# Kernel tuning notes

Hardware: AMD Instinct MI355X
Metric: run time of the kernel (lower is better)

Reference implementation:

```python
import jax, jax.numpy as jnp
import numpy as np

D_MODEL = 1024
NUM_HEADS = 16
HEAD_DIM = D_MODEL // NUM_HEADS  # 64
ROPE_THETA = 10000.0
SEQ_LEN = 4096
BATCH = 1


def apply_rope(x, positions, theta=ROPE_THETA):
    # x: [b, h, s, d], positions: [s]
    d = x.shape[-1]
    inv_freq = theta ** (-jnp.arange(0, d, 2, dtype=jnp.float32) / d)  # [d/2]
    angles = positions.astype(jnp.float32)[:, None] * inv_freq[None, :]  # [s, d/2]
    cos = jnp.cos(angles)  # [s, d/2]
    sin = jnp.sin(angles)
    x1 = x[..., 0::2]  # [b, h, s, d/2]
    x2 = x[..., 1::2]
    r1 = x1 * cos - x2 * sin
    r2 = x1 * sin + x2 * cos
    # interleave back to [..., d]
    out = jnp.stack([r1, r2], axis=-1).reshape(x.shape)
    return out.astype(x.dtype)


def setup_inputs() -> dict:
    key = jax.random.key(0)
    k_x, k_qkv, k_o = jax.random.split(key, 3)
    scale_in = 1.0 / np.sqrt(D_MODEL)
    return {
        "x": jax.random.normal(k_x, (BATCH, SEQ_LEN, D_MODEL), dtype=jnp.float32),
        "token_positions": jnp.arange(SEQ_LEN, dtype=jnp.int64 if jax.config.jax_enable_x64 else jnp.int32),
        "w_qkv": jax.random.normal(k_qkv, (3 * D_MODEL, D_MODEL), dtype=jnp.float32) * scale_in,
        "w_o": jax.random.normal(k_o, (D_MODEL, D_MODEL), dtype=jnp.float32) * scale_in,
    }


def reference(x, token_positions, w_qkv, w_o):
    b, s, _ = x.shape
    # QKV projection (Linear without bias, weight [out, in])
    x_qkv = jnp.einsum('bsd,ed->bse', x, w_qkv)  # [b, s, 3*d_model]
    # rearrange 'b s (three heads kv) -> three b heads s kv'
    x_qkv = x_qkv.reshape(b, s, 3, NUM_HEADS, HEAD_DIM)
    x_qkv = jnp.transpose(x_qkv, (2, 0, 3, 1, 4))  # [3, b, h, s, d]
    q, k, v = x_qkv[0], x_qkv[1], x_qkv[2]
    q = apply_rope(q, token_positions)
    k = apply_rope(k, token_positions)
    # scaled dot-product attention with causal mask
    scores = jnp.einsum('bhnd,bhmd->bhnm', q, k) / jnp.sqrt(jnp.float32(HEAD_DIM))
    causal = jnp.tril(jnp.ones((s, s), dtype=bool))  # [s, s]
    scores = jnp.where(causal[None, None], scores, jnp.float32(-jnp.inf))
    weights = jax.nn.softmax(scores, axis=-1)
    attn = jnp.einsum('bhnm,bhmd->bhnd', weights, v)  # [b, h, s, d]
    attn = jnp.transpose(attn, (0, 2, 1, 3)).reshape(b, s, NUM_HEADS * HEAD_DIM)
    return jnp.einsum('bsd,ed->bse', attn, w_o)
```

## Files before the change

### kernel.cpp

```cpp
#include <hip/hip_runtime.h>

#define SEQ 4096
#define DMODEL 1024
#define HEADS 16
#define HD 64
#define NQKV 3072

typedef __attribute__((ext_vector_type(8))) __bf16 bf16x8;
typedef __attribute__((ext_vector_type(4))) __bf16 bf16x4;
typedef __attribute__((ext_vector_type(8))) short short8;
typedef __attribute__((ext_vector_type(4))) float f32x4;

__device__ __forceinline__ unsigned short f2bf(float f) {
    unsigned u = __builtin_bit_cast(unsigned, f);
    return (unsigned short)((u + 0x7fffu + ((u >> 16) & 1u)) >> 16);
}
__device__ __forceinline__ float bf2f(unsigned short h) {
    return __builtin_bit_cast(float, (unsigned)h << 16);
}

__device__ __forceinline__ void gload16(const void* g, void* l) {
    __builtin_amdgcn_global_load_lds(
        (const __attribute__((address_space(1))) unsigned int*)g,
        (__attribute__((address_space(3))) unsigned int*)l, 16, 0, 0);
}

#define TS(qt, kh) (0x40 | ((kh) << 5) | (qt))
__device__ __constant__ unsigned char TASKS[48] = {
    TS(31,0), TS(31,1), TS(30,0), 15,
    TS(30,1), TS(29,0), TS(29,1), TS(28,0), 14,
    TS(28,1), TS(27,0), TS(27,1), TS(26,0), 13,
    TS(26,1), TS(25,0), TS(25,1), TS(24,0), 12,
    TS(24,1), TS(23,0), TS(23,1), TS(22,0), 11,
    TS(22,1), TS(21,0), TS(21,1), TS(20,0), 10,
    TS(20,1), TS(19,0), TS(19,1), TS(18,0), 9,
    TS(18,1), TS(17,0), TS(17,1), TS(16,0), 8,
    TS(16,1), 7,
    6, 5, 4, 3, 2, 1, 0
};

__global__ void f2bf_all(const float* __restrict__ x, const float* __restrict__ wqkv,
                         const float* __restrict__ wo, unsigned short* __restrict__ dst) {
    const int N0 = SEQ * DMODEL / 4;
    const int N1 = N0 + NQKV * DMODEL / 4;
    const int NT = N1 + DMODEL * DMODEL / 4;
    int i = blockIdx.x * 256 + threadIdx.x;
    int stride = gridDim.x * 256;
    for (; i < NT; i += stride) {
        const float4* src;
        if (i < N0)      src = reinterpret_cast<const float4*>(x) + i;
        else if (i < N1) src = reinterpret_cast<const float4*>(wqkv) + (i - N0);
        else             src = reinterpret_cast<const float4*>(wo) + (i - N1);
        float4 f = *src;
        ushort4 o;
        o.x = f2bf(f.x); o.y = f2bf(f.y); o.z = f2bf(f.z); o.w = f2bf(f.w);
        reinterpret_cast<ushort4*>(dst)[i] = o;
    }
}

template <int EPI>
__global__ __launch_bounds__(256) void gemm_bt(const unsigned short* __restrict__ A,
                                               const unsigned short* __restrict__ B,
                                               float* __restrict__ outF,
                                               unsigned short* __restrict__ outB,
                                               int M, int N, int K) {
    alignas(16) __shared__ unsigned short a_lds[2][128 * 32];
    alignas(16) __shared__ unsigned short b_lds[2][128 * 32];
    const int tid = threadIdx.x;
    const int wave = tid >> 6, lane = tid & 63;
    const int l16 = lane & 15, g = lane >> 4;
    const int wr = wave >> 1, wc = wave & 1;
    const int bm = blockIdx.x, bn = blockIdx.y;

    const int lrow = lane >> 2;
    const int lcol = (lane & 3) * 8;

    const unsigned short* Ag = A + (size_t)(bm * 128 + lrow) * K + lcol;
    const unsigned short* Bg = B + (size_t)(bn * 128 + lrow) * K + lcol;

    f32x4 acc[4][4] = {};
    const int NS = K / 32;

    auto STAGE = [&](int b, int ks) {
#pragma unroll
        for (int j = 0; j < 2; ++j) {
            int chunk = wave * 2 + j;
            gload16(Ag + (size_t)(chunk * 16) * K + ks * 32, a_lds[b] + chunk * 512);
            gload16(Bg + (size_t)(chunk * 16) * K + ks * 32, b_lds[b] + chunk * 512);
        }
    };

    STAGE(0, 0);

    for (int ks = 0; ks < NS; ++ks) {
        const int cur = ks & 1;
        asm volatile("s_waitcnt vmcnt(0)" ::: "memory");
        __builtin_amdgcn_s_barrier();
        if (ks + 1 < NS) STAGE(cur ^ 1, ks + 1);

        bf16x8 af[4], bfr[4];
#pragma unroll
        for (int m = 0; m < 4; ++m)
            af[m] = *reinterpret_cast<const bf16x8*>(a_lds[cur] + (wr * 64 + m * 16 + l16) * 32 + g * 8);
#pragma unroll
        for (int n = 0; n < 4; ++n)
            bfr[n] = *reinterpret_cast<const bf16x8*>(b_lds[cur] + (wc * 64 + n * 16 + l16) * 32 + g * 8);
        __builtin_amdgcn_s_setprio(1);
#pragma unroll
        for (int m = 0; m < 4; ++m)
#pragma unroll
            for (int n = 0; n < 4; ++n)
                acc[m][n] = __builtin_amdgcn_mfma_f32_16x16x32_bf16(af[m], bfr[n], acc[m][n], 0, 0, 0);
        __builtin_amdgcn_s_setprio(0);
    }

#pragma unroll
    for (int m = 0; m < 4; ++m)
#pragma unroll
        for (int n = 0; n < 4; ++n)
#pragma unroll
            for (int r = 0; r < 4; ++r) {
                int row = bm * 128 + wr * 64 + m * 16 + g * 4 + r;
                int col = bn * 128 + wc * 64 + n * 16 + l16;
                float v = acc[m][n][r];
                if (EPI == 0) {
                    int part = col >> 10;
                    int hd = col & 1023;
                    int h = hd >> 6, d = hd & 63;
                    outB[(size_t)((part * HEADS + h) * SEQ + row) * HD + d] = f2bf(v);
                } else {
                    outF[(size_t)row * N + col] = v;
                }
            }
}

__global__ __launch_bounds__(256) void rope_kernel(unsigned short* qkv, const int* __restrict__ pos) {
    int idx = blockIdx.x * 256 + threadIdx.x;
    int chunk = idx & 7;
    int row = idx >> 3;
    int s = row & (SEQ - 1);
    int ph = row >> 12;
    float p = (float)pos[s];
    float scale = (ph < HEADS) ? 0.125f * 1.4426950408889634f : 1.0f;
    unsigned short* base = qkv + ((size_t)ph * SEQ + s) * HD + chunk * 8;
    short8 v = *reinterpret_cast<short8*>(base);
    short8 o;
    const float k = -13.287712379549449f / 32.0f;
#pragma unroll
    for (int j = 0; j < 4; ++j) {
        int i = chunk * 4 + j;
        float ang = p * exp2f((float)i * k);
        float sn, cs;
        sincosf(ang, &sn, &cs);
        float x1 = bf2f((unsigned short)v[2 * j]);
        float x2 = bf2f((unsigned short)v[2 * j + 1]);
        o[2 * j]     = (short)f2bf((x1 * cs - x2 * sn) * scale);
        o[2 * j + 1] = (short)f2bf((x1 * sn + x2 * cs) * scale);
    }
    *reinterpret_cast<short8*>(base) = o;
}

__global__ __launch_bounds__(256) void transpose_v(const unsigned short* __restrict__ qkv,
                                                   unsigned short* __restrict__ vt) {
    const int st = blockIdx.x;
    const int h = blockIdx.y;
    __shared__ unsigned short tile[64][72];
    const unsigned short* Vg = qkv + (size_t)((2 * HEADS + h) * SEQ) * HD;
    const int tid = threadIdx.x;
#pragma unroll
    for (int j = 0; j < 2; ++j) {
        int b = (tid + j * 256) * 8;
        int row = b >> 6;
        int col = b & 63;
        short8 v = *reinterpret_cast<const short8*>(Vg + (size_t)(st * 64 + row) * HD + col);
#pragma unroll
        for (int i = 0; i < 8; ++i) tile[row][col + i] = (unsigned short)v[i];
    }
    __syncthreads();
#pragma unroll
    for (int j = 0; j < 2; ++j) {
        int b = (tid + j * 256) * 8;
        int d = b >> 6;
        int sc = b & 63;
        short8 o;
#pragma unroll
        for (int i = 0; i < 8; ++i) o[i] = (short)tile[sc + i][d];
        *reinterpret_cast<short8*>(vt + (size_t)(h * HD + d) * SEQ + st * 64 + sc) = o;
    }
}

__global__ __launch_bounds__(512) void attn_kernel(const unsigned short* __restrict__ qkv,
                                                   const unsigned short* __restrict__ vt,
                                                   unsigned short* __restrict__ attnout,
                                                   unsigned short* __restrict__ pO,
                                                   float* __restrict__ lmf) {
    const int bid = blockIdx.x;
    const int xcd = bid & 7;
    const int slot = bid >> 3;
    const int hloc = slot & 1;
    const unsigned char e = TASKS[slot >> 1];
    const int qtile = e & 31;
    const int khalf = (e >> 5) & 1;
    const bool isSplit = (e >> 6) != 0;
    const int T = qtile + 1, Hh = (T + 1) >> 1;
    const int k0 = isSplit ? (khalf ? Hh : 0) : 0;
    const int k1 = isSplit ? (khalf ? T : Hh) : T;
    const int h = xcd * 2 + hloc;

    const int tid = threadIdx.x;
    const int wave = tid >> 6, lane = tid & 63;
    const int l16 = lane & 15, g = lane >> 4;

    alignas(16) __shared__ unsigned short k_lds[2][128 * 64];
    alignas(16) __shared__ unsigned short v_lds[2][2][64 * 64];
    alignas(16) __shared__ unsigned short p_lds[8][16 * 64];

    const unsigned short* Qg = qkv + (size_t)((0 * HEADS + h) * SEQ) * HD;
    const unsigned short* Kg = qkv + (size_t)((1 * HEADS + h) * SEQ) * HD;
    const unsigned short* VTg = vt + (size_t)h * HD * SEQ;

    const int qbase = qtile * 128 + wave * 16;
    bf16x8 qf[2];
    qf[0] = *reinterpret_cast<const bf16x8*>(Qg + (size_t)(qbase + l16) * HD + g * 8);
    qf[1] = *reinterpret_cast<const bf16x8*>(Qg + (size_t)(qbase + l16) * HD + 32 + g * 8);

    bf16x8 ones;
#pragma unroll
    for (int j2 = 0; j2 < 8; ++j2) ones[j2] = (__bf16)1.0f;

    f32x4 o_acc[4] = {};
    f32x4 l_acc = {};
    float m_r = -1e30f;

    char* pwave = (char*)p_lds + wave * 2048;
    const int rsw = (l16 & 7) << 4;

    auto STAGE = [&](int b, int kt) {
#pragma unroll
        for (int i = 0; i < 2; ++i) {
            int base = wave * 2048 + i * 1024;
            int byte = base + lane * 16;
            int krow = byte >> 7;
            int kc8 = ((byte >> 4) & 7) ^ (krow & 7);
            gload16(Kg + (size_t)(kt * 128 + krow) * HD + kc8 * 8, (char*)k_lds[b] + base);
            int fr = byte >> 7;
            int h64 = fr >> 6, vd = fr & 63;
            int vc8 = ((byte >> 4) & 7) ^ (vd & 7);
            gload16(VTg + (size_t)vd * SEQ + kt * 128 + h64 * 64 + vc8 * 8,
                    (char*)v_lds[b] + base);
        }
    };

    STAGE(0, k0);

    for (int kt = k0; kt < k1; ++kt) {
        const int cur = (kt - k0) & 1;
        asm volatile("s_waitcnt vmcnt(0)" ::: "memory");
        __builtin_amdgcn_s_barrier();
        if (kt + 1 < k1) STAGE(cur ^ 1, kt + 1);

        const bool doB = (kt * 128 + 64) <= (qbase + 15);

        f32x4 s[8] = {};
        __builtin_amdgcn_s_setprio(1);
#pragma unroll
        for (int nt = 0; nt < 4; ++nt) {
            int row = nt * 16 + l16;
#pragma unroll
            for (int kk = 0; kk < 2; ++kk) {
                bf16x8 kf = *reinterpret_cast<const bf16x8*>(
                    (char*)k_lds[cur] + row * 128 + (((kk * 4 + g) << 4) ^ rsw));
                s[nt] = __builtin_amdgcn_mfma_f32_16x16x32_bf16(kf, qf[kk], s[nt], 0, 0, 0);
            }
        }
        if (doB) {
#pragma unroll
            for (int nt = 0; nt < 4; ++nt) {
                int row = 64 + nt * 16 + l16;
#pragma unroll
                for (int kk = 0; kk < 2; ++kk) {
                    bf16x8 kf = *reinterpret_cast<const bf16x8*>(
                        (char*)k_lds[cur] + row * 128 + (((kk * 4 + g) << 4) ^ rsw));
                    s[4 + nt] = __builtin_amdgcn_mfma_f32_16x16x32_bf16(kf, qf[kk], s[4 + nt], 0, 0, 0);
                }
            }
        }
        __builtin_amdgcn_s_setprio(0);

        if (kt * 128 + 127 > qbase) {
            int qrow = qbase + l16;
#pragma unroll
            for (int nt = 0; nt < 4; ++nt)
#pragma unroll
                for (int r = 0; r < 4; ++r) {
                    int kv = kt * 128 + nt * 16 + g * 4 + r;
                    if (kv > qrow) s[nt][r] = -1e30f;
                    if (kv + 64 > qrow) s[4 + nt][r] = -1e30f;
                }
        }

        f32x4 m4;
#pragma unroll
        for (int r = 0; r < 4; ++r) {
            float a = fmaxf(fmaxf(s[0][r], s[1][r]), fmaxf(s[2][r], s[3][r]));
            float b = fmaxf(fmaxf(s[4][r], s[5][r]), fmaxf(s[6][r], s[7][r]));
            m4[r] = fmaxf(a, b);
        }
        float mx = fmaxf(fmaxf(m4[0], m4[1]), fmaxf(m4[2], m4[3]));
        mx = fmaxf(mx, __shfl_xor(mx, 16));
        mx = fmaxf(mx, __shfl_xor(mx, 32));

        if (__any(mx > m_r + 8.0f)) {
            float mnew = fmaxf(m_r, mx);
            float alpha = __builtin_amdgcn_exp2f(m_r - mnew);
            m_r = mnew;
#pragma unroll
            for (int dt = 0; dt < 4; ++dt)
#pragma unroll
                for (int r = 0; r < 4; ++r) o_acc[dt][r] *= alpha;
            l_acc[0] *= alpha;
        }

#pragma unroll
        for (int i = 0; i < 8; ++i)
#pragma unroll
            for (int r = 0; r < 4; ++r) s[i][r] = __builtin_amdgcn_exp2f(s[i][r] - m_r);

        __builtin_amdgcn_s_setprio(1);
#pragma unroll
        for (int h64 = 0; h64 < 2; ++h64) {
            if (h64 && !doB) break;
#pragma unroll
            for (int nt = 0; nt < 4; ++nt) {
                bf16x4 pb;
#pragma unroll
                for (int r = 0; r < 4; ++r) pb[r] = (__bf16)s[h64 * 4 + nt][r];
                *reinterpret_cast<bf16x4*>(pwave + l16 * 128 + ((nt * 32 + g * 8) ^ rsw)) = pb;
            }
            bf16x8 pfrag[2];
#pragma unroll
            for (int kk = 0; kk < 2; ++kk)
                pfrag[kk] = *reinterpret_cast<const bf16x8*>(
                    pwave + l16 * 128 + (((kk * 4 + g) << 4) ^ rsw));

#pragma unroll
            for (int dt = 0; dt < 4; ++dt) {
                int row = dt * 16 + l16;
#pragma unroll
                for (int kk = 0; kk < 2; ++kk) {
                    bf16x8 vf = *reinterpret_cast<const bf16x8*>(
                        (char*)v_lds[cur][h64] + row * 128 + (((kk * 4 + g) << 4) ^ rsw));
                    o_acc[dt] = __builtin_amdgcn_mfma_f32_16x16x32_bf16(vf, pfrag[kk], o_acc[dt], 0, 0, 0);
                }
            }
            l_acc = __builtin_amdgcn_mfma_f32_16x16x32_bf16(ones, pfrag[0], l_acc, 0, 0, 0);
            l_acc = __builtin_amdgcn_mfma_f32_16x16x32_bf16(ones, pfrag[1], l_acc, 0, 0, 0);
        }
        __builtin_amdgcn_s_setprio(0);
    }

    const int ql = wave * 16 + l16;
    if (isSplit) {
        int sidx = (h * 16 + (qtile - 16)) * 2 + khalf;
        unsigned short* Op = pO + (size_t)sidx * 8192;
#pragma unroll
        for (int dt = 0; dt < 4; ++dt) {
            ushort4 ov;
            ov.x = f2bf(o_acc[dt][0]);
            ov.y = f2bf(o_acc[dt][1]);
            ov.z = f2bf(o_acc[dt][2]);
            ov.w = f2bf(o_acc[dt][3]);
            *reinterpret_cast<ushort4*>(Op + ql * 64 + dt * 16 + g * 4) = ov;
        }
        if (g == 0) {
            lmf[sidx * 256 + ql] = l_acc[0];
            lmf[sidx * 256 + 128 + ql] = m_r;
        }
    } else {
        float inv = 1.0f / l_acc[0];
        int q = qtile * 128 + ql;
#pragma unroll
        for (int dt = 0; dt < 4; ++dt) {
            ushort4 ov;
            ov.x = f2bf(o_acc[dt][0] * inv);
            ov.y = f2bf(o_acc[dt][1] * inv);
            ov.z = f2bf(o_acc[dt][2] * inv);
            ov.w = f2bf(o_acc[dt][3] * inv);
            *reinterpret_cast<ushort4*>(attnout + (size_t)q * DMODEL + h * HD + dt * 16 + g * 4) = ov;
        }
    }
}

__global__ __launch_bounds__(256) void merge_kernel(const unsigned short* __restrict__ pO,
                                                    const float* __restrict__ lmf,
                                                    unsigned short* __restrict__ attnout) {
    int idx = blockIdx.x * 256 + threadIdx.x;
    if (idx >= 16 * 16 * 1024) return;
    int h = idx / (16 * 1024);
    int r = idx % (16 * 1024);
    int qt = r >> 10;
    int rr = r & 1023;
    int q = rr >> 3, d8 = rr & 7;

    int s0 = (h * 16 + qt) * 2;
    float l0 = lmf[s0 * 256 + q],       m0 = lmf[s0 * 256 + 128 + q];
    float l1 = lmf[(s0 + 1) * 256 + q], m1 = lmf[(s0 + 1) * 256 + 128 + q];
    float m = fmaxf(m0, m1);
    float a0 = __builtin_amdgcn_exp2f(m0 - m), a1 = __builtin_amdgcn_exp2f(m1 - m);
    float L = l0 * a0 + l1 * a1;
    float c0 = a0 / L, c1 = a1 / L;

    const unsigned short* O0 = pO + (size_t)s0 * 8192 + q * 64 + d8 * 8;
    const unsigned short* O1 = O0 + 8192;
    short8 v0 = *reinterpret_cast<const short8*>(O0);
    short8 v1 = *reinterpret_cast<const short8*>(O1);
    short8 o;
#pragma unroll
    for (int j = 0; j < 8; ++j) {
        float val = bf2f((unsigned short)v0[j]) * c0 + bf2f((unsigned short)v1[j]) * c1;
        o[j] = (short)f2bf(val);
    }
    int qtile = qt + 16;
    *reinterpret_cast<short8*>(attnout + (size_t)(qtile * 128 + q) * DMODEL + h * HD + d8 * 8) = o;
}

extern "C" void kernel_launch(void* const* d_in, const int* in_sizes, int n_in,
                              void* d_out, int out_size, void* d_ws, size_t ws_size,
                              hipStream_t stream) {
    const float* x = (const float*)d_in[0];
    const int* pos = (const int*)d_in[1];
    const float* wqkv = (const float*)d_in[2];
    const float* wo = (const float*)d_in[3];
    float* out = (float*)d_out;

    unsigned short* xb = (unsigned short*)d_ws;
    unsigned short* wqkvb = xb + (size_t)SEQ * DMODEL;
    unsigned short* wob = wqkvb + (size_t)NQKV * DMODEL;
    unsigned short* qkvp = wob + (size_t)DMODEL * DMODEL;
    unsigned short* vt = qkvp + (size_t)3 * HEADS * SEQ * HD;
    unsigned short* attnb = vt + (size_t)HEADS * HD * SEQ;

    char* sbase = (char*)d_ws;
    float* lmf = (float*)sbase;
    unsigned short* pO = (unsigned short*)(sbase + (1 << 20));

    f2bf_all<<<2048, 256, 0, stream>>>(x, wqkv, wo, xb);

    dim3 g1(SEQ / 128, NQKV / 128);
    gemm_bt<0><<<g1, 256, 0, stream>>>(xb, wqkvb, nullptr, qkvp, SEQ, NQKV, DMODEL);

    rope_kernel<<<(2 * HEADS * SEQ * 8) / 256, 256, 0, stream>>>(qkvp, pos);
    transpose_v<<<dim3(SEQ / 64, HEADS), 256, 0, stream>>>(qkvp, vt);

    attn_kernel<<<768, 512, 0, stream>>>(qkvp, vt, attnb, pO, lmf);
    merge_kernel<<<(16 * 16 * 1024 + 255) / 256, 256, 0, stream>>>(pO, lmf, attnb);

    dim3 g2(SEQ / 128, DMODEL / 128);
    gemm_bt<1><<<g2, 256, 0, stream>>>(attnb, wob, out, nullptr, SEQ, DMODEL, DMODEL);
}
```

Measured before the change: 148.6 us.

## Switch attention to 32x32x16 MFMA with register-resident P and 4-wave blocks

Rewrites the attention inner loop to use 32x32x16 bf16 MFMA tiles, with each wave owning 32 query rows and the block shrunk from 8 to 4 waves. The probability matrix is now packed to bf16 with v_cvt_pk_bf16 and rearranged across lane halves with shuffles, replacing the LDS round trip for P. The row sum is computed with VALU adds and shuffles instead of an MFMA against a ones vector. This cuts LDS traffic and MFMA instruction count, at the cost of fewer waves per block, higher register pressure and a per-64-key-chunk softmax rescale.

```diff
diff --git a/kernel.cpp b/kernel.cpp
--- a/kernel.cpp
+++ b/kernel.cpp
@@ -10,6 +10,8 @@
 typedef __attribute__((ext_vector_type(4))) __bf16 bf16x4;
 typedef __attribute__((ext_vector_type(8))) short short8;
 typedef __attribute__((ext_vector_type(4))) float f32x4;
+typedef __attribute__((ext_vector_type(16))) float f32x16;
+typedef __attribute__((ext_vector_type(4))) unsigned int u32x4;
 
 __device__ __forceinline__ unsigned short f2bf(float f) {
     unsigned u = __builtin_bit_cast(unsigned, f);
@@ -17,6 +19,11 @@
 }
 __device__ __forceinline__ float bf2f(unsigned short h) {
     return __builtin_bit_cast(float, (unsigned)h << 16);
+}
+__device__ __forceinline__ unsigned cvt_pk_bf16(float lo, float hi) {
+    unsigned r;
+    asm("v_cvt_pk_bf16_f32 %0, %1, %2" : "=v"(r) : "v"(lo), "v"(hi));
+    return r;
 }
 
 __device__ __forceinline__ void gload16(const void* g, void* l) {
@@ -189,7 +196,7 @@
     }
 }
 
-__global__ __launch_bounds__(512) void attn_kernel(const unsigned short* __restrict__ qkv,
+__global__ __launch_bounds__(256) void attn_kernel(const unsigned short* __restrict__ qkv,
                                                    const unsigned short* __restrict__ vt,
                                                    unsigned short* __restrict__ attnout,
                                                    unsigned short* __restrict__ pO,
@@ -209,36 +216,32 @@
 
     const int tid = threadIdx.x;
     const int wave = tid >> 6, lane = tid & 63;
-    const int l16 = lane & 15, g = lane >> 4;
+    const int l32 = lane & 31, hi = lane >> 5;
 
     alignas(16) __shared__ unsigned short k_lds[2][128 * 64];
     alignas(16) __shared__ unsigned short v_lds[2][2][64 * 64];
-    alignas(16) __shared__ unsigned short p_lds[8][16 * 64];
 
     const unsigned short* Qg = qkv + (size_t)((0 * HEADS + h) * SEQ) * HD;
     const unsigned short* Kg = qkv + (size_t)((1 * HEADS + h) * SEQ) * HD;
     const unsigned short* VTg = vt + (size_t)h * HD * SEQ;
 
-    const int qbase = qtile * 128 + wave * 16;
-    bf16x8 qf[2];
-    qf[0] = *reinterpret_cast<const bf16x8*>(Qg + (size_t)(qbase + l16) * HD + g * 8);
-    qf[1] = *reinterpret_cast<const bf16x8*>(Qg + (size_t)(qbase + l16) * HD + 32 + g * 8);
-
-    bf16x8 ones;
-#pragma unroll
-    for (int j2 = 0; j2 < 8; ++j2) ones[j2] = (__bf16)1.0f;
-
-    f32x4 o_acc[4] = {};
-    f32x4 l_acc = {};
-    float m_r = -1e30f;
-
-    char* pwave = (char*)p_lds + wave * 2048;
-    const int rsw = (l16 & 7) << 4;
+    const int qbase = qtile * 128 + wave * 32;
+    const int qrow = qbase + l32;
+
+    bf16x8 qf[4];
+#pragma unroll
+    for (int dg = 0; dg < 4; ++dg)
+        qf[dg] = *reinterpret_cast<const bf16x8*>(Qg + (size_t)qrow * HD + dg * 16 + hi * 8);
+
+    f32x16 oa[2] = {};
+    float m_r = -1e30f, l_r = 0.f;
+
+    const int rsw = (l32 & 7) << 4;
 
     auto STAGE = [&](int b, int kt) {
 #pragma unroll
-        for (int i = 0; i < 2; ++i) {
-            int base = wave * 2048 + i * 1024;
+        for (int i = 0; i < 4; ++i) {
+            int base = wave * 4096 + i * 1024;
             int byte = base + lane * 16;
             int krow = byte >> 7;
             int kc8 = ((byte >> 4) & 7) ^ (krow & 7);
@@ -259,135 +262,135 @@
         __builtin_amdgcn_s_barrier();
         if (kt + 1 < k1) STAGE(cur ^ 1, kt + 1);
 
-        const bool doB = (kt * 128 + 64) <= (qbase + 15);
-
-        f32x4 s[8] = {};
-        __builtin_amdgcn_s_setprio(1);
-#pragma unroll
-        for (int nt = 0; nt < 4; ++nt) {
-            int row = nt * 16 + l16;
-#pragma unroll
-            for (int kk = 0; kk < 2; ++kk) {
-                bf16x8 kf = *reinterpret_cast<const bf16x8*>(
-                    (char*)k_lds[cur] + row * 128 + (((kk * 4 + g) << 4) ^ rsw));
-                s[nt] = __builtin_amdgcn_mfma_f32_16x16x32_bf16(kf, qf[kk], s[nt], 0, 0, 0);
-            }
+#pragma unroll
+        for (int hh = 0; hh < 2; ++hh) {
+            if (hh && (kt * 128 + 64) > (qbase + 31)) break;
+
+            f32x16 s[2] = {};
+            __builtin_amdgcn_s_setprio(1);
+#pragma unroll
+            for (int g = 0; g < 2; ++g) {
+                int row = hh * 64 + g * 32 + l32;
+#pragma unroll
+                for (int dg = 0; dg < 4; ++dg) {
+                    bf16x8 kf = *reinterpret_cast<const bf16x8*>(
+                        (char*)k_lds[cur] + row * 128 + ((dg * 32 + hi * 16) ^ rsw));
+                    s[g] = __builtin_amdgcn_mfma_f32_32x32x16_bf16(kf, qf[dg], s[g], 0, 0, 0);
+                }
+            }
+            __builtin_amdgcn_s_setprio(0);
+
+            if (kt * 128 + hh * 64 + 63 > qbase) {
+#pragma unroll
+                for (int g = 0; g < 2; ++g)
+#pragma unroll
+                    for (int r = 0; r < 16; ++r) {
+                        int kv = kt * 128 + hh * 64 + g * 32 + (r & 3) + 8 * (r >> 2) + 4 * hi;
+                        if (kv > qrow) s[g][r] = -1e30f;
+                    }
+            }
+
+            float ma = -1e30f, mb = -1e30f, mc = -1e30f, md = -1e30f;
+#pragma unroll
+            for (int r = 0; r < 16; r += 4) {
+                ma = fmaxf(ma, fmaxf(s[0][r], s[1][r]));
+                mb = fmaxf(mb, fmaxf(s[0][r + 1], s[1][r + 1]));
+                mc = fmaxf(mc, fmaxf(s[0][r + 2], s[1][r + 2]));
+                md = fmaxf(md, fmaxf(s[0][r + 3], s[1][r + 3]));
+            }
+            float mx = fmaxf(fmaxf(ma, mb), fmaxf(mc, md));
+            mx = fmaxf(mx, __shfl_xor(mx, 32));
+
+            if (__any(mx > m_r + 8.0f)) {
+                float mnew = fmaxf(m_r, mx);
+                float alpha = __builtin_amdgcn_exp2f(m_r - mnew);
+                m_r = mnew;
+#pragma unroll
+                for (int r = 0; r < 16; ++r) { oa[0][r] *= alpha; oa[1][r] *= alpha; }
+                l_r *= alpha;
+            }
+
+#pragma unroll
+            for (int g = 0; g < 2; ++g)
+#pragma unroll
+                for (int r = 0; r < 16; ++r) s[g][r] = __builtin_amdgcn_exp2f(s[g][r] - m_r);
+
+            float ra = 0.f, rb = 0.f;
+#pragma unroll
+            for (int r = 0; r < 16; r += 2) {
+                ra += s[0][r] + s[1][r];
+                rb += s[0][r + 1] + s[1][r + 1];
+            }
+            float rs = ra + rb;
+            rs += __shfl_xor(rs, 32);
+            l_r += rs;
+
+            __builtin_amdgcn_s_setprio(1);
+#pragma unroll
+            for (int g = 0; g < 2; ++g) {
+                u32x4 pfw[2];
+#pragma unroll
+                for (int u = 0; u < 2; ++u) {
+                    unsigned wA = cvt_pk_bf16(s[g][8 * u + 0], s[g][8 * u + 1]);
+                    unsigned wC = cvt_pk_bf16(s[g][8 * u + 2], s[g][8 * u + 3]);
+                    unsigned wB = cvt_pk_bf16(s[g][8 * u + 4], s[g][8 * u + 5]);
+                    unsigned wD = cvt_pk_bf16(s[g][8 * u + 6], s[g][8 * u + 7]);
+                    unsigned wAx = __shfl_xor((int)wA, 32), wBx = __shfl_xor((int)wB, 32);
+                    unsigned wCx = __shfl_xor((int)wC, 32), wDx = __shfl_xor((int)wD, 32);
+                    pfw[u][0] = hi ? wBx : wA;
+                    pfw[u][1] = hi ? wDx : wC;
+                    pfw[u][2] = hi ? wB : wAx;
+                    pfw[u][3] = hi ? wD : wCx;
+                }
+#pragma unroll
+                for (int u = 0; u < 2; ++u) {
+                    bf16x8 pf = __builtin_bit_cast(bf16x8, pfw[u]);
+                    int ks = g * 2 + u;
+#pragma unroll
+                    for (int dg = 0; dg < 2; ++dg) {
+                        bf16x8 vf = *reinterpret_cast<const bf16x8*>(
+                            (char*)v_lds[cur][hh] + (dg * 32 + l32) * 128 + ((ks * 32 + hi * 16) ^ rsw));
+                        oa[dg] = __builtin_amdgcn_mfma_f32_32x32x16_bf16(vf, pf, oa[dg], 0, 0, 0);
+                    }
+                }
+            }
+            __builtin_amdgcn_s_setprio(0);
         }
-        if (doB) {
-#pragma unroll
-            for (int nt = 0; nt < 4; ++nt) {
-                int row = 64 + nt * 16 + l16;
-#pragma unroll
-                for (int kk = 0; kk < 2; ++kk) {
-                    bf16x8 kf = *reinterpret_cast<const bf16x8*>(
-                        (char*)k_lds[cur] + row * 128 + (((kk * 4 + g) << 4) ^ rsw));
-                    s[4 + nt] = __builtin_amdgcn_mfma_f32_16x16x32_bf16(kf, qf[kk], s[4 + nt], 0, 0, 0);
-                }
-            }
-        }
-        __builtin_amdgcn_s_setprio(0);
-
-        if (kt * 128 + 127 > qbase) {
-            int qrow = qbase + l16;
-#pragma unroll
-            for (int nt = 0; nt < 4; ++nt)
-#pragma unroll
-                for (int r = 0; r < 4; ++r) {
-                    int kv = kt * 128 + nt * 16 + g * 4 + r;
-                    if (kv > qrow) s[nt][r] = -1e30f;
-                    if (kv + 64 > qrow) s[4 + nt][r] = -1e30f;
-                }
-        }
-
-        f32x4 m4;
-#pragma unroll
-        for (int r = 0; r < 4; ++r) {
-            float a = fmaxf(fmaxf(s[0][r], s[1][r]), fmaxf(s[2][r], s[3][r]));
-            float b = fmaxf(fmaxf(s[4][r], s[5][r]), fmaxf(s[6][r], s[7][r]));
-            m4[r] = fmaxf(a, b);
-        }
-        float mx = fmaxf(fmaxf(m4[0], m4[1]), fmaxf(m4[2], m4[3]));
-        mx = fmaxf(mx, __shfl_xor(mx, 16));
-        mx = fmaxf(mx, __shfl_xor(mx, 32));
-
-        if (__any(mx > m_r + 8.0f)) {
-            float mnew = fmaxf(m_r, mx);
-            float alpha = __builtin_amdgcn_exp2f(m_r - mnew);
-            m_r = mnew;
-#pragma unroll
-            for (int dt = 0; dt < 4; ++dt)
-#pragma unroll
-                for (int r = 0; r < 4; ++r) o_acc[dt][r] *= alpha;
-            l_acc[0] *= alpha;
-        }
-
-#pragma unroll
-        for (int i = 0; i < 8; ++i)
-#pragma unroll
-            for (int r = 0; r < 4; ++r) s[i][r] = __builtin_amdgcn_exp2f(s[i][r] - m_r);
-
-        __builtin_amdgcn_s_setprio(1);
-#pragma unroll
-        for (int h64 = 0; h64 < 2; ++h64) {
-            if (h64 && !doB) break;
-#pragma unroll
-            for (int nt = 0; nt < 4; ++nt) {
-                bf16x4 pb;
-#pragma unroll
-                for (int r = 0; r < 4; ++r) pb[r] = (__bf16)s[h64 * 4 + nt][r];
-                *reinterpret_cast<bf16x4*>(pwave + l16 * 128 + ((nt * 32 + g * 8) ^ rsw)) = pb;
-            }
-            bf16x8 pfrag[2];
-#pragma unroll
-            for (int kk = 0; kk < 2; ++kk)
-                pfrag[kk] = *reinterpret_cast<const bf16x8*>(
-                    pwave + l16 * 128 + (((kk * 4 + g) << 4) ^ rsw));
-
-#pragma unroll
-            for (int dt = 0; dt < 4; ++dt) {
-                int row = dt * 16 + l16;
-#pragma unroll
-                for (int kk = 0; kk < 2; ++kk) {
-                    bf16x8 vf = *reinterpret_cast<const bf16x8*>(
-                        (char*)v_lds[cur][h64] + row * 128 + (((kk * 4 + g) << 4) ^ rsw));
-                    o_acc[dt] = __builtin_amdgcn_mfma_f32_16x16x32_bf16(vf, pfrag[kk], o_acc[dt], 0, 0, 0);
-                }
-            }
-            l_acc = __builtin_amdgcn_mfma_f32_16x16x32_bf16(ones, pfrag[0], l_acc, 0, 0, 0);
-            l_acc = __builtin_amdgcn_mfma_f32_16x16x32_bf16(ones, pfrag[1], l_acc, 0, 0, 0);
-        }
-        __builtin_amdgcn_s_setprio(0);
-    }
-
-    const int ql = wave * 16 + l16;
+    }
+
+    const int ql = wave * 32 + l32;
     if (isSplit) {
         int sidx = (h * 16 + (qtile - 16)) * 2 + khalf;
         unsigned short* Op = pO + (size_t)sidx * 8192;
 #pragma unroll
-        for (int dt = 0; dt < 4; ++dt) {
-            ushort4 ov;
-            ov.x = f2bf(o_acc[dt][0]);
-            ov.y = f2bf(o_acc[dt][1]);
-            ov.z = f2bf(o_acc[dt][2]);
-            ov.w = f2bf(o_acc[dt][3]);
-            *reinterpret_cast<ushort4*>(Op + ql * 64 + dt * 16 + g * 4) = ov;
-        }
-        if (g == 0) {
-            lmf[sidx * 256 + ql] = l_acc[0];
+        for (int dg = 0; dg < 2; ++dg)
+#pragma unroll
+            for (int rq = 0; rq < 4; ++rq) {
+                ushort4 ov;
+                ov.x = f2bf(oa[dg][4 * rq + 0]);
+                ov.y = f2bf(oa[dg][4 * rq + 1]);
+                ov.z = f2bf(oa[dg][4 * rq + 2]);
+                ov.w = f2bf(oa[dg][4 * rq + 3]);
+                *reinterpret_cast<ushort4*>(Op + ql * 64 + dg * 32 + 8 * rq + 4 * hi) = ov;
+            }
+        if (hi == 0) {
+            lmf[sidx * 256 + ql] = l_r;
             lmf[sidx * 256 + 128 + ql] = m_r;
         }
     } else {
-        float inv = 1.0f / l_acc[0];
-        int q = qtile * 128 + ql;
-#pragma unroll
-        for (int dt = 0; dt < 4; ++dt) {
-            ushort4 ov;
-            ov.x = f2bf(o_acc[dt][0] * inv);
-            ov.y = f2bf(o_acc[dt][1] * inv);
-            ov.z = f2bf(o_acc[dt][2] * inv);
-            ov.w = f2bf(o_acc[dt][3] * inv);
-            *reinterpret_cast<ushort4*>(attnout + (size_t)q * DMODEL + h * HD + dt * 16 + g * 4) = ov;
-        }
+        float inv = 1.0f / l_r;
+        unsigned short* orow = attnout + (size_t)(qtile * 128 + ql) * DMODEL + h * HD;
+#pragma unroll
+        for (int dg = 0; dg < 2; ++dg)
+#pragma unroll
+            for (int rq = 0; rq < 4; ++rq) {
+                ushort4 ov;
+                ov.x = f2bf(oa[dg][4 * rq + 0] * inv);
+                ov.y = f2bf(oa[dg][4 * rq + 1] * inv);
+                ov.z = f2bf(oa[dg][4 * rq + 2] * inv);
+                ov.w = f2bf(oa[dg][4 * rq + 3] * inv);
+                *reinterpret_cast<ushort4*>(orow + dg * 32 + 8 * rq + 4 * hi) = ov;
+            }
     }
 }
 
@@ -452,7 +455,7 @@
     rope_kernel<<<(2 * HEADS * SEQ * 8) / 256, 256, 0, stream>>>(qkvp, pos);
     transpose_v<<<dim3(SEQ / 64, HEADS), 256, 0, stream>>>(qkvp, vt);
 
-    attn_kernel<<<768, 512, 0, stream>>>(qkvp, vt, attnb, pO, lmf);
+    attn_kernel<<<768, 256, 0, stream>>>(qkvp, vt, attnb, pO, lmf);
     merge_kernel<<<(16 * 16 * 1024 + 255) / 256, 256, 0, stream>>>(pO, lmf, attnb);
 
     dim3 g2(SEQ / 128, DMODEL / 128);
```

Result: slower. 158.0 us (+6.4%).
